# Kernel tuning notes

Hardware: AMD Instinct MI355X
Metric: run time of the kernel (lower is better)

Reference implementation:

```python
import jax, jax.numpy as jnp
import numpy as np

CHANNELS = 3
SCALE = 0.25


def _gaussian_kernel():
    # Mirrors AntiAliasInterpolation2d.__init__
    sigma = (1.0 / SCALE - 1.0) / 2.0            # 1.5
    ka = int(round(sigma * 4))                   # 6 -> kernel_size 13
    k1 = np.exp(-np.arange(-ka, ka + 1, dtype=np.float32) ** 2 / (2.0 * sigma ** 2))
    k2 = np.outer(k1, k1)
    k2 = k2 / k2.sum()
    # depthwise weight: (C_out=C, C_in/groups=1, kh, kw)
    return jnp.asarray(np.tile(k2[None, None], (CHANNELS, 1, 1, 1)).astype(np.float32))


def setup_inputs() -> dict:
    key = jax.random.key(0)
    x = jax.random.normal(key, (32, 3, 512, 512), dtype=jnp.float32)
    weight = _gaussian_kernel()
    return {"x": x, "weight": weight}


def _bilinear_resize(x, out_h, out_w):
    # PyTorch F.interpolate(mode='bilinear', align_corners=False)
    N, C, H, W = x.shape

    def idx(n_in, n_out):
        src = (jnp.arange(n_out, dtype=jnp.float32) + 0.5) * (n_in / n_out) - 0.5
        src = jnp.clip(src, 0.0, n_in - 1)
        i0 = jnp.floor(src).astype(jnp.int32)
        i1 = jnp.minimum(i0 + 1, n_in - 1)
        w = src - i0.astype(jnp.float32)
        return i0, i1, w

    h0, h1, wh = idx(H, out_h)
    w0, w1, ww = idx(W, out_w)
    # interpolate rows then cols
    xh = x[:, :, h0, :] * (1.0 - wh)[:, None] + x[:, :, h1, :] * wh[:, None]
    return xh[:, :, :, w0] * (1.0 - ww) + xh[:, :, :, w1] * ww


def reference(x, weight):
    ka = weight.shape[-1] // 2  # kernel odd -> pad ka on all sides (ka == kb)
    xp = jnp.pad(x, ((0, 0), (0, 0), (ka, ka), (ka, ka)))
    blurred = jax.lax.conv_general_dilated(
        xp, weight,
        window_strides=(1, 1), padding='VALID',
        dimension_numbers=('NCHW', 'OIHW', 'NCHW'),
        feature_group_count=x.shape[1],
    )
    H, W = blurred.shape[2], blurred.shape[3]
    return _bilinear_resize(blurred, int(H * SCALE), int(W * SCALE))
```

## Files before the change

### kernel.cpp

```cpp
#include <hip/hip_runtime.h>
#include <math.h>


#define H 512
#define W 512
#define OH 128
#define OW 128
#define NC 96
#define TAPS 14
#define TI 16
#define NTILES (OH / TI)
#define ROWS (4 * (TI - 1) + TAPS)
#define LSTRIDE (W + W / 32)

struct G14 { float g[TAPS]; };

__global__ __launch_bounds__(256) void aa_interp_kernel(
    const float* __restrict__ x, float* __restrict__ out, G14 gk) {
    const int bid = blockIdx.x;
    const int tb  = bid & (NTILES - 1);
    const int nc  = bid >> 3;
    const int t   = threadIdx.x;

    const float* img = x + (size_t)nc * H * W;
    const int r_start = tb * (4 * TI) - 5;

    float2 acc[TI];
#pragma unroll
    for (int io = 0; io < TI; ++io) acc[io] = make_float2(0.f, 0.f);

#pragma unroll
    for (int k = 0; k < ROWS; ++k) {
        const int r = r_start + k;
        float2 v = make_float2(0.f, 0.f);
        if (r >= 0 && r < H)
            v = reinterpret_cast<const float2*>(img + (size_t)r * W)[t];
        const int lo = (k >= TAPS) ? ((k - TAPS + 4) >> 2) : 0;
        const int hi = ((k >> 2) < (TI - 1)) ? (k >> 2) : (TI - 1);
#pragma unroll
        for (int io = lo; io <= hi; ++io) {
            const float g = gk.g[k - 4 * io];
            acc[io].x += g * v.x;
            acc[io].y += g * v.y;
        }
    }

    __shared__ float lds[TI * LSTRIDE];
    {
        const int c0 = 2 * t, c1 = 2 * t + 1;
        const int a0 = c0 + (c0 >> 5), a1 = c1 + (c1 >> 5);
#pragma unroll
        for (int io = 0; io < TI; ++io) {
            lds[io * LSTRIDE + a0] = acc[io].x;
            lds[io * LSTRIDE + a1] = acc[io].y;
        }
    }
    __syncthreads();

    const int io = t >> 4;
    const int j0 = (t & 15) * 8;
    const float* lrow = lds + io * LSTRIDE;
    const int cb = 4 * j0 - 5;

    float win[42];
#pragma unroll
    for (int w = 0; w < 42; ++w) {
        const int c = cb + w;
        float v = 0.f;
        if (c >= 0 && c < W) v = lrow[c + (c >> 5)];
        win[w] = v;
    }

    float res[8];
#pragma unroll
    for (int jj = 0; jj < 8; ++jj) {
        float s = 0.f;
#pragma unroll
        for (int v = 0; v < TAPS; ++v) s += gk.g[v] * win[4 * jj + v];
        res[jj] = s;
    }

    float* op = out + ((size_t)nc * OH + tb * TI + io) * OW + j0;
    reinterpret_cast<float4*>(op)[0] = make_float4(res[0], res[1], res[2], res[3]);
    reinterpret_cast<float4*>(op)[1] = make_float4(res[4], res[5], res[6], res[7]);
}

extern "C" void kernel_launch(void* const* d_in, const int* in_sizes, int n_in,
                              void* d_out, int out_size, void* d_ws, size_t ws_size,
                              hipStream_t stream) {
    const float* x = (const float*)d_in[0];
    float* out = (float*)d_out;

    G14 gk;
    {
        double k1[13], s = 0.0;
        for (int d = 0; d < 13; ++d) {
            double dd = d - 6;
            k1[d] = exp(-(dd * dd) / (2.0 * 1.5 * 1.5));
            s += k1[d];
        }
        for (int u = 0; u < TAPS; ++u) {
            double lo = (u - 1 >= 0 && u - 1 < 13) ? k1[u - 1] : 0.0;
            double hi = (u < 13) ? k1[u] : 0.0;
            gk.g[u] = (float)(0.5 * (lo + hi) / s);
        }
    }

    const int blocks = NC * NTILES;
    aa_interp_kernel<<<blocks, 256, 0, stream>>>(x, out, gk);
}
```

Measured before the change: 24.49 us.

## Use 512 threads per block, one column each, and remap block order

Doubles threads per block so each thread handles one input column in the vertical pass and four output pixels in the horizontal pass, instead of two columns and eight pixels. Block indices are also permuted so consecutive hardware blocks come from different image slices. The aim is more memory-level parallelism and lower register pressure per thread. The cost is narrower scalar loads in place of float2 loads, and less work per thread to amortise overhead.

```diff
diff --git a/kernel.cpp b/kernel.cpp
--- a/kernel.cpp
+++ b/kernel.cpp
@@ -10,70 +10,63 @@
 #define TAPS 14
 #define TI 16
 #define NTILES (OH / TI)
+#define GRID (NC * NTILES)
 #define ROWS (4 * (TI - 1) + TAPS)
 #define LSTRIDE (W + W / 32)
 
 struct G14 { float g[TAPS]; };
 
-__global__ __launch_bounds__(256) void aa_interp_kernel(
+__global__ __launch_bounds__(512) void aa_interp_kernel(
     const float* __restrict__ x, float* __restrict__ out, G14 gk) {
-    const int bid = blockIdx.x;
-    const int tb  = bid & (NTILES - 1);
-    const int nc  = bid >> 3;
-    const int t   = threadIdx.x;
+    const int bid  = (blockIdx.x & 7) * (GRID / 8) + (blockIdx.x >> 3);
+    const int tb   = bid & (NTILES - 1);
+    const int nc   = bid >> 3;
+    const int t    = threadIdx.x;
 
     const float* img = x + (size_t)nc * H * W;
     const int r_start = tb * (4 * TI) - 5;
 
-    float2 acc[TI];
+    float acc[TI];
 #pragma unroll
-    for (int io = 0; io < TI; ++io) acc[io] = make_float2(0.f, 0.f);
+    for (int io = 0; io < TI; ++io) acc[io] = 0.f;
 
 #pragma unroll
     for (int k = 0; k < ROWS; ++k) {
         const int r = r_start + k;
-        float2 v = make_float2(0.f, 0.f);
-        if (r >= 0 && r < H)
-            v = reinterpret_cast<const float2*>(img + (size_t)r * W)[t];
+        float v = 0.f;
+        if (r >= 0 && r < H) v = img[(size_t)r * W + t];
         const int lo = (k >= TAPS) ? ((k - TAPS + 4) >> 2) : 0;
         const int hi = ((k >> 2) < (TI - 1)) ? (k >> 2) : (TI - 1);
 #pragma unroll
-        for (int io = lo; io <= hi; ++io) {
-            const float g = gk.g[k - 4 * io];
-            acc[io].x += g * v.x;
-            acc[io].y += g * v.y;
-        }
+        for (int io = lo; io <= hi; ++io) acc[io] += gk.g[k - 4 * io] * v;
     }
 
     __shared__ float lds[TI * LSTRIDE];
     {
-        const int c0 = 2 * t, c1 = 2 * t + 1;
-        const int a0 = c0 + (c0 >> 5), a1 = c1 + (c1 >> 5);
+        const int a = t + (t >> 5);
 #pragma unroll
-        for (int io = 0; io < TI; ++io) {
-            lds[io * LSTRIDE + a0] = acc[io].x;
-            lds[io * LSTRIDE + a1] = acc[io].y;
-        }
+        for (int io = 0; io < TI; ++io) lds[io * LSTRIDE + a] = acc[io];
     }
     __syncthreads();
 
-    const int io = t >> 4;
-    const int j0 = (t & 15) * 8;
+    const int io = t >> 5;
+    const int jg = t & 31;
+    const int j0 = jg * 4;
     const float* lrow = lds + io * LSTRIDE;
     const int cb = 4 * j0 - 5;
 
-    float win[42];
+    float win[26];
 #pragma unroll
-    for (int w = 0; w < 42; ++w) {
+    for (int w = 0; w < 26; ++w) {
         const int c = cb + w;
         float v = 0.f;
         if (c >= 0 && c < W) v = lrow[c + (c >> 5)];
         win[w] = v;
     }
 
-    float res[8];
+    float res[4];
 #pragma unroll
-    for (int jj = 0; jj < 8; ++jj) {
+    for (int jj = 0; jj < 4; ++jj) {
         float s = 0.f;
 #pragma unroll
         for (int v = 0; v < TAPS; ++v) s += gk.g[v] * win[4 * jj + v];
@@ -82,7 +75,6 @@
 
     float* op = out + ((size_t)nc * OH + tb * TI + io) * OW + j0;
     reinterpret_cast<float4*>(op)[0] = make_float4(res[0], res[1], res[2], res[3]);
-    reinterpret_cast<float4*>(op)[1] = make_float4(res[4], res[5], res[6], res[7]);
 }
 
 extern "C" void kernel_launch(void* const* d_in, const int* in_sizes, int n_in,
@@ -106,6 +98,5 @@
         }
     }
 
-    const int blocks = NC * NTILES;
-    aa_interp_kernel<<<blocks, 256, 0, stream>>>(x, out, gk);
+    aa_interp_kernel<<<GRID, 512, 0, stream>>>(x, out, gk);
 }
```

After: 21.87 us, median of 2. 10.7% less time.
